# Kernel optimization log

Hardware: AMD Instinct MI355X
Metric: run time of the kernel (lower is better)

## Reference

```python
import jax, jax.numpy as jnp
import numpy as np

B, T, D_MODEL = 2, 2048, 1024
H, D_HEAD, R = 16, 64, 16
CAUSAL = True


def setup_inputs() -> dict:
    key = jax.random.key(0)
    ks = jax.random.split(key, 6)
    return {
        "x": jax.random.normal(ks[0], (B, T, D_MODEL), dtype=jnp.float32),
        "W_qkv": jax.random.normal(ks[1], (D_MODEL, 3 * D_MODEL), dtype=jnp.float32) * 0.02,
        "W_q_lsr": jax.random.normal(ks[2], (H, D_HEAD, R), dtype=jnp.float32) * 0.1,
        "W_k_lsr": jax.random.normal(ks[3], (H, D_HEAD, R), dtype=jnp.float32) * 0.1,
        "core": jax.random.normal(ks[4], (H, R), dtype=jnp.float32),
        "W_o": jax.random.normal(ks[5], (D_MODEL, D_MODEL), dtype=jnp.float32) * 0.02,
    }


def reference(x, W_qkv, W_q_lsr, W_k_lsr, core, W_o):
    Bx, Tx, D = x.shape
    Hh, Dh, Rr = W_q_lsr.shape
    # Fused QKV projection, then split heads -> (B, H, T, D_head)
    qkv = x @ W_qkv  # (B, T, 3D)
    q, k, v = jnp.split(qkv, 3, axis=-1)
    q = q.reshape(Bx, Tx, Hh, Dh).transpose(0, 2, 1, 3)
    k = k.reshape(Bx, Tx, Hh, Dh).transpose(0, 2, 1, 3)
    v = v.reshape(Bx, Tx, Hh, Dh).transpose(0, 2, 1, 3)
    # Low-rank (LSR) projections of q and k; core + 1/sqrt(R) scaling on q side
    scale = 1.0 / jnp.sqrt(jnp.asarray(max(Rr, 1), dtype=jnp.float32))
    q_lr = jnp.einsum('bhtd,hdr->bhtr', q, W_q_lsr) * core[None, :, None, :] * scale
    k_lr = jnp.einsum('bhtd,hdr->bhtr', k, W_k_lsr)
    # Low-rank scores (B, H, T, T)
    scores = jnp.einsum('bhir,bhjr->bhij', q_lr, k_lr)
    if CAUSAL:
        mask = jnp.tril(jnp.ones((Tx, Tx), dtype=bool))
        scores = jnp.where(mask[None, None], scores, -jnp.inf)
    attn = jax.nn.softmax(scores, axis=-1)
    out = jnp.einsum('bhij,bhjd->bhid', attn, v)  # (B, H, T, D_head)
    out = out.transpose(0, 2, 1, 3).reshape(Bx, Tx, D)
    return out @ W_o
```

## Files before the change

kernel.cpp:

```cpp
#include <hip/hip_runtime.h>
#include <hip/hip_bf16.h>

#define BB 2
#define TT 2048
#define DD 1024
#define HH 16
#define DH 64
#define RR 16
#define BT (BB*TT)
#define BH (BB*HH)
#define D3 (3*DD)
#define NC 1536

typedef __bf16 bf16x8 __attribute__((ext_vector_type(8)));
typedef float f32x4 __attribute__((ext_vector_type(4)));
typedef short short4v __attribute__((ext_vector_type(4)));

__device__ __forceinline__ float bf2f(unsigned short u) {
  unsigned int v = ((unsigned int)u) << 16;
  return __builtin_bit_cast(float, v);
}
__device__ __forceinline__ unsigned short f2bf(float f) {
  unsigned int x = __builtin_bit_cast(unsigned int, f);
  unsigned int r = x + 0x7fffu + ((x >> 16) & 1u);
  return (unsigned short)(r >> 16);
}
__device__ __forceinline__ short4v pack_bf16x4(float a, float b, float c, float d) {
  uint2 u;
  u.x = (unsigned)f2bf(a) | ((unsigned)f2bf(b) << 16);
  u.y = (unsigned)f2bf(c) | ((unsigned)f2bf(d) << 16);
  return __builtin_bit_cast(short4v, u);
}

#define NEG_BIG (-1e30f)

__device__ __forceinline__ void async_copy16(const void* g, void* l) {
  __builtin_amdgcn_global_load_lds((const __attribute__((address_space(1))) void*)g,
                                   (__attribute__((address_space(3))) void*)l, 16, 0, 0);
}

__global__ __launch_bounds__(256) void cvt_f32_bf16(const float* __restrict__ in,
                                                    unsigned short* __restrict__ out,
                                                    int n) {
  int i = (blockIdx.x * 256 + threadIdx.x) * 8;
  if (i >= n) return;
  float4 a = *(const float4*)&in[i];
  float4 b = *(const float4*)&in[i + 4];
  unsigned short t[8] = {f2bf(a.x), f2bf(a.y), f2bf(a.z), f2bf(a.w),
                         f2bf(b.x), f2bf(b.y), f2bf(b.z), f2bf(b.w)};
  *(uint4*)&out[i] = *(const uint4*)t;
}

__global__ __launch_bounds__(256) void transpose_cvt(const float* __restrict__ in,
                                                     unsigned short* __restrict__ out,
                                                     int R, int C, int coff) {
  __shared__ float tile[32][33];
  const int tx = threadIdx.x, ty = threadIdx.y;
  const int x = blockIdx.x * 32 + tx;
  const int y0 = blockIdx.y * 32;
#pragma unroll
  for (int i = 0; i < 32; i += 8)
    tile[ty + i][tx] = in[(size_t)(y0 + ty + i) * C + coff + x];
  __syncthreads();
  const int xo = y0 + tx;
  const int yo0 = blockIdx.x * 32;
#pragma unroll
  for (int i = 0; i < 32; i += 8)
    out[(size_t)(yo0 + ty + i) * R + xo] = f2bf(tile[tx][ty + i]);
}

__global__ __launch_bounds__(256) void build_lsr(const float* __restrict__ Wqkv,
                                                 const float* __restrict__ Wql,
                                                 const float* __restrict__ Wkl,
                                                 const float* __restrict__ core,
                                                 unsigned short* __restrict__ Wcomb_t) {
  const int d0 = blockIdx.x * 64, h = blockIdx.y, tid = threadIdx.x;
  __shared__ float Aq[64][65], Ak[64][65], Lq[64][16], Lk[64][16], cs[16];
#pragma unroll
  for (int p = 0; p < 16; p++) {
    int idx = p * 256 + tid, dd = idx >> 6, e = idx & 63;
    Aq[dd][e] = Wqkv[(size_t)(d0 + dd) * D3 + h * 64 + e];
    Ak[dd][e] = Wqkv[(size_t)(d0 + dd) * D3 + DD + h * 64 + e];
  }
#pragma unroll
  for (int p = 0; p < 4; p++) {
    int idx = p * 256 + tid, e = idx >> 4, r = idx & 15;
    Lq[e][r] = Wql[h * 1024 + e * 16 + r];
    Lk[e][r] = Wkl[h * 1024 + e * 16 + r];
  }
  if (tid < 16) cs[tid] = core[h * 16 + tid];
  __syncthreads();
  const int dd = tid & 63, rg = tid >> 6;
  float aq[4] = {}, ak[4] = {};
  for (int e = 0; e < 64; e++) {
    float xq = Aq[dd][e], xk = Ak[dd][e];
#pragma unroll
    for (int j = 0; j < 4; j++) {
      aq[j] += xq * Lq[e][rg * 4 + j];
      ak[j] += xk * Lk[e][rg * 4 + j];
    }
  }
#pragma unroll
  for (int j = 0; j < 4; j++) {
    int r = rg * 4 + j;
    Wcomb_t[(size_t)(1024 + h * 16 + r) * DD + d0 + dd] =
        f2bf(aq[j] * cs[r] * (0.25f * 1.4426950408889634f));
    Wcomb_t[(size_t)(1280 + h * 16 + r) * DD + d0 + dd] = f2bf(ak[j]);
  }
}

__device__ __forceinline__ void gemm64_core(const unsigned short* __restrict__ A,
                                            const unsigned short* __restrict__ Bt,
                                            int K, int bm, int bn,
                                            int tid, int g, int c, int wm, int wn,
                                            f32x4 acc[2][4]) {
  __shared__ __attribute__((aligned(16))) unsigned short As[2][64 * 32];
  __shared__ __attribute__((aligned(16))) unsigned short Bs[2][128 * 32];
  const int e0 = tid * 8;
  const int r0 = e0 >> 5, q0 = e0 & 31;
  const unsigned short* Arow = &A[(size_t)(bm * 64 + r0) * K + q0];
  const unsigned short* Brow0 = &Bt[(size_t)(bn * 128 + r0) * K + q0];
  const unsigned short* Brow1 = &Bt[(size_t)(bn * 128 + 64 + r0) * K + q0];
  async_copy16(Arow, &As[0][e0]);
  async_copy16(Brow0, &Bs[0][e0]);
  async_copy16(Brow1, &Bs[0][2048 + e0]);
  __syncthreads();
  const int nsteps = K >> 5;
#pragma unroll 2
  for (int t = 0; t < nsteps; t++) {
    const int cur = t & 1, nxt = cur ^ 1;
    if (t + 1 < nsteps) {
      const int k1 = (t + 1) << 5;
      async_copy16(Arow + k1, &As[nxt][e0]);
      async_copy16(Brow0 + k1, &Bs[nxt][e0]);
      async_copy16(Brow1 + k1, &Bs[nxt][2048 + e0]);
    }
    bf16x8 af[2];
#pragma unroll
    for (int mt = 0; mt < 2; mt++)
      af[mt] = *(const bf16x8*)&As[cur][(wm * 32 + mt * 16 + c) * 32 + g * 8];
#pragma unroll
    for (int nt = 0; nt < 4; nt++) {
      bf16x8 bf = *(const bf16x8*)&Bs[cur][(wn * 64 + nt * 16 + c) * 32 + g * 8];
#pragma unroll
      for (int mt = 0; mt < 2; mt++)
        acc[mt][nt] = __builtin_amdgcn_mfma_f32_16x16x32_bf16(af[mt], bf, acc[mt][nt], 0, 0, 0);
    }
    __syncthreads();
  }
}

__global__ __launch_bounds__(256) void gemm64_f32(const unsigned short* __restrict__ A,
                                                  const unsigned short* __restrict__ Bt,
                                                  float* __restrict__ C,
                                                  int M, int N, int K) {
  const int tid = threadIdx.x, lane = tid & 63;
  const int g = lane >> 4, c = lane & 15;
  const int wid = tid >> 6, wm = wid >> 1, wn = wid & 1;
  const int bm = blockIdx.y, bn = blockIdx.x;
  f32x4 acc[2][4] = {};
  gemm64_core(A, Bt, K, bm, bn, tid, g, c, wm, wn, acc);
#pragma unroll
  for (int mt = 0; mt < 2; mt++)
#pragma unroll
    for (int nt = 0; nt < 4; nt++)
#pragma unroll
      for (int r = 0; r < 4; r++) {
        int row = bm * 64 + wm * 32 + mt * 16 + g * 4 + r;
        int col = bn * 128 + wn * 64 + nt * 16 + c;
        C[(size_t)row * N + col] = acc[mt][nt][r];
      }
}

__global__ __launch_bounds__(256) void gemm_fused(const unsigned short* __restrict__ A,
                                                  const unsigned short* __restrict__ Bt,
                                                  unsigned short* __restrict__ qls,
                                                  unsigned short* __restrict__ klr,
                                                  unsigned short* __restrict__ vt,
                                                  int M, int N, int K) {
  const int tid = threadIdx.x, lane = tid & 63;
  const int g = lane >> 4, c = lane & 15;
  const int wid = tid >> 6, wm = wid >> 1, wn = wid & 1;
  const int bm = blockIdx.y, bn = blockIdx.x;
  f32x4 acc[2][4] = {};
  gemm64_core(A, Bt, K, bm, bn, tid, g, c, wm, wn, acc);
#pragma unroll
  for (int mt = 0; mt < 2; mt++)
#pragma unroll
    for (int nt = 0; nt < 4; nt++) {
      int colb = bn * 128 + wn * 64 + nt * 16;
      int tg0 = bm * 64 + wm * 32 + mt * 16 + g * 4;
      int b = tg0 >> 11, t0 = tg0 & 2047;
      if (colb < 1024) {
        int h = colb >> 6, d = (colb & 63) + c;
        uint2 pk = __builtin_bit_cast(uint2, pack_bf16x4(acc[mt][nt][0], acc[mt][nt][1],
                                                         acc[mt][nt][2], acc[mt][nt][3]));
        size_t idx = (size_t)(b * 16 + h) * (TT / 4) * 256 + (size_t)(t0 >> 2) * 256 + d * 4;
        *(uint2*)&vt[idx] = pk;
      } else if (colb < 1280) {
        int h = (colb - 1024) >> 4;
        size_t base = (size_t)(b * 16 + h) * TT;
#pragma unroll
        for (int r = 0; r < 4; r++)
          qls[(base + t0 + r) * 16 + c] = f2bf(acc[mt][nt][r]);
      } else {
        int h = (colb - 1280) >> 4;
        size_t base = (size_t)(b * 16 + h) * TT;
#pragma unroll
        for (int r = 0; r < 4; r++)
          klr[(base + t0 + r) * 16 + c] = f2bf(acc[mt][nt][r]);
      }
    }
}

__global__ __launch_bounds__(256, 3) void flash_lsr(const unsigned short* __restrict__ qls,
                                                    const unsigned short* __restrict__ klr,
                                                    const unsigned short* __restrict__ vt,
                                                    unsigned short* __restrict__ attn) {
  const int bh = blockIdx.x & 31, b = bh >> 4, h = bh & 15;
  const int qt = 31 - (blockIdx.x >> 5);
  const int tid = threadIdx.x, lane = tid & 63, w = tid >> 6;
  const int g = lane >> 4, c = lane & 15;
  const int q0 = qt * 64, jmax = qt >> 1;

  __shared__ __attribute__((aligned(16))) unsigned short Ks[2][128 * 20];
  __shared__ __attribute__((aligned(16))) unsigned short Vs[2][32 * 264];

  const size_t qbase = (size_t)bh * TT;
  const short4v qf = __builtin_bit_cast(short4v,
      *(const uint2*)&qls[(qbase + q0 + w * 16 + c) * 16 + g * 4]);
  const int qg = q0 + w * 16 + c;
  float mi = NEG_BIG, li = 0.f;
  f32x4 oa[4] = {};
  const f32x4 zero = {0.f, 0.f, 0.f, 0.f};
  const size_t kb = (size_t)bh * TT * 16;
  const size_t vb = (size_t)bh * TT * 64;
  const int srcl = g * 20;

  uint4 kr = *(const uint4*)&klr[kb + tid * 8];
  uint4 vr[4];
#pragma unroll
  for (int p = 0; p < 4; p++)
    vr[p] = *(const uint4*)&vt[vb + (p * 256 + tid) * 8];

  int p = 0;
  f32x4 s[8];
  for (int jt = 0; jt <= jmax; jt++) {
    *(uint4*)&Ks[p][(tid >> 1) * 20 + (tid & 1) * 8] = kr;
#pragma unroll
    for (int q = 0; q < 4; q++) {
      int e = (q * 256 + tid) * 8;
      *(uint4*)&Vs[p][(e >> 8) * 264 + (e & 255)] = vr[q];
    }
    __syncthreads();
    if (jt < jmax) {
      kr = *(const uint4*)&klr[kb + (size_t)(jt + 1) * 2048 + tid * 8];
      const unsigned short* vp = &vt[vb + (size_t)(jt + 1) * 8192];
#pragma unroll
      for (int q = 0; q < 4; q++)
        vr[q] = *(const uint4*)&vp[(q * 256 + tid) * 8];
    }
    const unsigned short* Kb = Ks[p];
#pragma unroll
    for (int nt = 0; nt < 8; nt++) {
      short4v kf = __builtin_bit_cast(short4v, *(const uint2*)&Kb[(nt * 16 + c) * 20 + g * 4]);
      s[nt] = __builtin_amdgcn_mfma_f32_16x16x16bf16_1k(kf, qf, zero, 0, 0, 0);
    }
    if (jt == jmax) {
#pragma unroll
      for (int nt = 0; nt < 8; nt++)
#pragma unroll
        for (int r = 0; r < 4; r++) {
          int jg = jt * 128 + nt * 16 + g * 4 + r;
          if (jg > qg) s[nt][r] = NEG_BIG;
        }
    }
    f32x4 vm = s[0];
#pragma unroll
    for (int nt = 1; nt < 8; nt++)
#pragma unroll
      for (int r = 0; r < 4; r++) vm[r] = fmaxf(vm[r], s[nt][r]);
    float rm = fmaxf(fmaxf(vm[0], vm[1]), fmaxf(vm[2], vm[3]));
    rm = fmaxf(rm, __shfl_xor(rm, 16, 64));
    rm = fmaxf(rm, __shfl_xor(rm, 32, 64));
    float mnew = fmaxf(mi, rm);
    float alpha = __builtin_amdgcn_exp2f(mi - mnew);
    mi = mnew;
    f32x4 vs = zero;
#pragma unroll
    for (int nt = 0; nt < 8; nt++)
#pragma unroll
      for (int r = 0; r < 4; r++) {
        float pv = __builtin_amdgcn_exp2f(s[nt][r] - mnew);
        s[nt][r] = pv;
        vs[r] += pv;
      }
    float rs = (vs[0] + vs[1]) + (vs[2] + vs[3]);
    rs += __shfl_xor(rs, 16, 64);
    rs += __shfl_xor(rs, 32, 64);
    li = li * alpha + rs;
    float av[4];
#pragma unroll
    for (int r = 0; r < 4; r++) av[r] = __shfl(alpha, srcl + r, 64);
#pragma unroll
    for (int nd = 0; nd < 4; nd++)
#pragma unroll
      for (int r = 0; r < 4; r++) oa[nd][r] *= av[r];
    const unsigned short* Vb = Vs[p];
#pragma unroll
    for (int kc = 0; kc < 8; kc++) {
      short4v af = pack_bf16x4(s[kc][0], s[kc][1], s[kc][2], s[kc][3]);
#pragma unroll
      for (int nd = 0; nd < 4; nd++) {
        uint2 vv = *(const uint2*)&Vb[(kc * 4 + g) * 264 + (nd * 16 + c) * 4];
        short4v vf = __builtin_bit_cast(short4v, vv);
        oa[nd] = __builtin_amdgcn_mfma_f32_16x16x16bf16_1k(af, vf, oa[nd], 0, 0, 0);
      }
    }
    p ^= 1;
  }

  float inv = 1.f / li;
  float iv[4];
#pragma unroll
  for (int r = 0; r < 4; r++) iv[r] = __shfl(inv, srcl + r, 64);
#pragma unroll
  for (int r = 0; r < 4; r++) {
    size_t rowb = ((size_t)b * TT + q0 + w * 16 + g * 4 + r) * DD + h * 64;
#pragma unroll
    for (int nd = 0; nd < 4; nd++)
      attn[rowb + nd * 16 + c] = f2bf(oa[nd][r] * iv[r]);
  }
}

extern "C" void kernel_launch(void* const* d_in, const int* in_sizes, int n_in,
                              void* d_out, int out_size, void* d_ws, size_t ws_size,
                              hipStream_t stream) {
  const float* x      = (const float*)d_in[0];
  const float* W_qkv  = (const float*)d_in[1];
  const float* W_qlsr = (const float*)d_in[2];
  const float* W_klsr = (const float*)d_in[3];
  const float* core   = (const float*)d_in[4];
  const float* W_o    = (const float*)d_in[5];
  float* out = (float*)d_out;

  char* ws = (char*)d_ws;
  unsigned short* x_bf    = (unsigned short*)ws; ws += (size_t)BT * DD * 2;
  unsigned short* Wcomb_t = (unsigned short*)ws; ws += (size_t)NC * DD * 2;
  unsigned short* Wo_t    = (unsigned short*)ws; ws += (size_t)DD * DD * 2;
  unsigned short* qls     = (unsigned short*)ws; ws += (size_t)BH * TT * 16 * 2;
  unsigned short* klr     = (unsigned short*)ws; ws += (size_t)BH * TT * 16 * 2;
  unsigned short* vt      = (unsigned short*)ws; ws += (size_t)BH * TT * 64 * 2;
  unsigned short* attn    = (unsigned short*)ws; ws += (size_t)BT * DD * 2;

  cvt_f32_bf16<<<(BT * DD) / (256 * 8), 256, 0, stream>>>(x, x_bf, BT * DD);
  transpose_cvt<<<dim3(32, 32), dim3(32, 8), 0, stream>>>(W_o, Wo_t, DD, DD, 0);
  transpose_cvt<<<dim3(32, 32), dim3(32, 8), 0, stream>>>(W_qkv, Wcomb_t, DD, D3, 2048);
  build_lsr<<<dim3(16, 16), 256, 0, stream>>>(W_qkv, W_qlsr, W_klsr, core, Wcomb_t);
  gemm_fused<<<dim3(NC / 128, BT / 64), 256, 0, stream>>>(x_bf, Wcomb_t, qls, klr, vt, BT, NC, DD);
  flash_lsr<<<dim3(32 * BH), 256, 0, stream>>>(qls, klr, vt, attn);
  gemm64_f32<<<dim3(DD / 128, BT / 64), 256, 0, stream>>>(attn, Wo_t, out, BT, DD, DD);
}
```

Before: 188.4 us.

## Fuse prep kernels into one launch and transpose PV MFMA to drop shuffles

Merges the x conversion, the two weight transposes and the LSR weight build into a single launch that branches on block index, removing three launch gaps. In the flash kernel the PV MFMA operands are swapped so each lane owns whole rows of the output. This removes the cross-lane shuffles for the alpha rescale and the final normalisation, and lets the output be written as packed 4-element stores. It also switches to hardware bf16 conversion for packing. The fused prep kernel allocates the larger shared-memory footprint for every block, which may lower occupancy on the simple conversion blocks.

```diff
diff --git a/kernel.cpp b/kernel.cpp
--- a/kernel.cpp
+++ b/kernel.cpp
@@ -13,6 +13,7 @@
 #define NC 1536
 
 typedef __bf16 bf16x8 __attribute__((ext_vector_type(8)));
+typedef __bf16 bf16x4 __attribute__((ext_vector_type(4)));
 typedef float f32x4 __attribute__((ext_vector_type(4)));
 typedef short short4v __attribute__((ext_vector_type(4)));
 
@@ -31,6 +32,10 @@
   u.y = (unsigned)f2bf(c) | ((unsigned)f2bf(d) << 16);
   return __builtin_bit_cast(short4v, u);
 }
+__device__ __forceinline__ short4v pack4_cvt(float a, float b, float c, float d) {
+  bf16x4 v = {(__bf16)a, (__bf16)b, (__bf16)c, (__bf16)d};
+  return __builtin_bit_cast(short4v, v);
+}
 
 #define NEG_BIG (-1e30f)
 
@@ -39,73 +44,74 @@
                                    (__attribute__((address_space(3))) void*)l, 16, 0, 0);
 }
 
-__global__ __launch_bounds__(256) void cvt_f32_bf16(const float* __restrict__ in,
-                                                    unsigned short* __restrict__ out,
-                                                    int n) {
-  int i = (blockIdx.x * 256 + threadIdx.x) * 8;
-  if (i >= n) return;
-  float4 a = *(const float4*)&in[i];
-  float4 b = *(const float4*)&in[i + 4];
-  unsigned short t[8] = {f2bf(a.x), f2bf(a.y), f2bf(a.z), f2bf(a.w),
-                         f2bf(b.x), f2bf(b.y), f2bf(b.z), f2bf(b.w)};
-  *(uint4*)&out[i] = *(const uint4*)t;
-}
-
-__global__ __launch_bounds__(256) void transpose_cvt(const float* __restrict__ in,
-                                                     unsigned short* __restrict__ out,
-                                                     int R, int C, int coff) {
+__global__ __launch_bounds__(256) void prep_fused(const float* __restrict__ x,
+                                                  const float* __restrict__ Wqkv,
+                                                  const float* __restrict__ Wql,
+                                                  const float* __restrict__ Wkl,
+                                                  const float* __restrict__ core,
+                                                  const float* __restrict__ Wo,
+                                                  unsigned short* __restrict__ x_bf,
+                                                  unsigned short* __restrict__ Wcomb_t,
+                                                  unsigned short* __restrict__ Wo_t) {
   __shared__ float tile[32][33];
-  const int tx = threadIdx.x, ty = threadIdx.y;
-  const int x = blockIdx.x * 32 + tx;
-  const int y0 = blockIdx.y * 32;
-#pragma unroll
-  for (int i = 0; i < 32; i += 8)
-    tile[ty + i][tx] = in[(size_t)(y0 + ty + i) * C + coff + x];
-  __syncthreads();
-  const int xo = y0 + tx;
-  const int yo0 = blockIdx.x * 32;
-#pragma unroll
-  for (int i = 0; i < 32; i += 8)
-    out[(size_t)(yo0 + ty + i) * R + xo] = f2bf(tile[tx][ty + i]);
-}
-
-__global__ __launch_bounds__(256) void build_lsr(const float* __restrict__ Wqkv,
-                                                 const float* __restrict__ Wql,
-                                                 const float* __restrict__ Wkl,
-                                                 const float* __restrict__ core,
-                                                 unsigned short* __restrict__ Wcomb_t) {
-  const int d0 = blockIdx.x * 64, h = blockIdx.y, tid = threadIdx.x;
   __shared__ float Aq[64][65], Ak[64][65], Lq[64][16], Lk[64][16], cs[16];
-#pragma unroll
-  for (int p = 0; p < 16; p++) {
-    int idx = p * 256 + tid, dd = idx >> 6, e = idx & 63;
-    Aq[dd][e] = Wqkv[(size_t)(d0 + dd) * D3 + h * 64 + e];
-    Ak[dd][e] = Wqkv[(size_t)(d0 + dd) * D3 + DD + h * 64 + e];
-  }
-#pragma unroll
-  for (int p = 0; p < 4; p++) {
-    int idx = p * 256 + tid, e = idx >> 4, r = idx & 15;
-    Lq[e][r] = Wql[h * 1024 + e * 16 + r];
-    Lk[e][r] = Wkl[h * 1024 + e * 16 + r];
-  }
-  if (tid < 16) cs[tid] = core[h * 16 + tid];
-  __syncthreads();
-  const int dd = tid & 63, rg = tid >> 6;
-  float aq[4] = {}, ak[4] = {};
-  for (int e = 0; e < 64; e++) {
-    float xq = Aq[dd][e], xk = Ak[dd][e];
+  const int bid = blockIdx.x, tid = threadIdx.x;
+  if (bid < 2048) {
+    int i = (bid * 256 + tid) * 8;
+    float4 a = *(const float4*)&x[i];
+    float4 b = *(const float4*)&x[i + 4];
+    unsigned short t[8] = {f2bf(a.x), f2bf(a.y), f2bf(a.z), f2bf(a.w),
+                           f2bf(b.x), f2bf(b.y), f2bf(b.z), f2bf(b.w)};
+    *(uint4*)&x_bf[i] = *(const uint4*)t;
+  } else if (bid < 4096) {
+    const float* in; unsigned short* out; int C, coff, lb;
+    if (bid < 3072) { in = Wo;   out = Wo_t;    C = DD; coff = 0;    lb = bid - 2048; }
+    else            { in = Wqkv; out = Wcomb_t; C = D3; coff = 2048; lb = bid - 3072; }
+    const int tx = tid & 31, ty = tid >> 5;
+    const int bx = lb & 31, by = lb >> 5;
+    const int xx = bx * 32 + tx, y0 = by * 32;
+#pragma unroll
+    for (int i = 0; i < 32; i += 8)
+      tile[ty + i][tx] = in[(size_t)(y0 + ty + i) * C + coff + xx];
+    __syncthreads();
+    const int xo = y0 + tx, yo0 = bx * 32;
+#pragma unroll
+    for (int i = 0; i < 32; i += 8)
+      out[(size_t)(yo0 + ty + i) * DD + xo] = f2bf(tile[tx][ty + i]);
+  } else {
+    const int l = bid - 4096;
+    const int d0 = (l & 15) * 64, h = l >> 4;
+#pragma unroll
+    for (int p = 0; p < 16; p++) {
+      int idx = p * 256 + tid, dd = idx >> 6, e = idx & 63;
+      Aq[dd][e] = Wqkv[(size_t)(d0 + dd) * D3 + h * 64 + e];
+      Ak[dd][e] = Wqkv[(size_t)(d0 + dd) * D3 + DD + h * 64 + e];
+    }
+#pragma unroll
+    for (int p = 0; p < 4; p++) {
+      int idx = p * 256 + tid, e = idx >> 4, r = idx & 15;
+      Lq[e][r] = Wql[h * 1024 + e * 16 + r];
+      Lk[e][r] = Wkl[h * 1024 + e * 16 + r];
+    }
+    if (tid < 16) cs[tid] = core[h * 16 + tid];
+    __syncthreads();
+    const int dd = tid & 63, rg = tid >> 6;
+    float aq[4] = {}, ak[4] = {};
+    for (int e = 0; e < 64; e++) {
+      float xq = Aq[dd][e], xk = Ak[dd][e];
+#pragma unroll
+      for (int j = 0; j < 4; j++) {
+        aq[j] += xq * Lq[e][rg * 4 + j];
+        ak[j] += xk * Lk[e][rg * 4 + j];
+      }
+    }
 #pragma unroll
     for (int j = 0; j < 4; j++) {
-      aq[j] += xq * Lq[e][rg * 4 + j];
-      ak[j] += xk * Lk[e][rg * 4 + j];
-    }
-  }
-#pragma unroll
-  for (int j = 0; j < 4; j++) {
-    int r = rg * 4 + j;
-    Wcomb_t[(size_t)(1024 + h * 16 + r) * DD + d0 + dd] =
-        f2bf(aq[j] * cs[r] * (0.25f * 1.4426950408889634f));
-    Wcomb_t[(size_t)(1280 + h * 16 + r) * DD + d0 + dd] = f2bf(ak[j]);
+      int r = rg * 4 + j;
+      Wcomb_t[(size_t)(1024 + h * 16 + r) * DD + d0 + dd] =
+          f2bf(aq[j] * cs[r] * (0.25f * 1.4426950408889634f));
+      Wcomb_t[(size_t)(1280 + h * 16 + r) * DD + d0 + dd] = f2bf(ak[j]);
+    }
   }
 }
 
@@ -235,7 +241,6 @@
   const f32x4 zero = {0.f, 0.f, 0.f, 0.f};
   const size_t kb = (size_t)bh * TT * 16;
   const size_t vb = (size_t)bh * TT * 64;
-  const int srcl = g * 20;
 
   uint4 kr = *(const uint4*)&klr[kb + tid * 8];
   uint4 vr[4];
@@ -299,37 +304,31 @@
     rs += __shfl_xor(rs, 16, 64);
     rs += __shfl_xor(rs, 32, 64);
     li = li * alpha + rs;
-    float av[4];
-#pragma unroll
-    for (int r = 0; r < 4; r++) av[r] = __shfl(alpha, srcl + r, 64);
 #pragma unroll
     for (int nd = 0; nd < 4; nd++)
 #pragma unroll
-      for (int r = 0; r < 4; r++) oa[nd][r] *= av[r];
+      for (int r = 0; r < 4; r++) oa[nd][r] *= alpha;
     const unsigned short* Vb = Vs[p];
 #pragma unroll
     for (int kc = 0; kc < 8; kc++) {
-      short4v af = pack_bf16x4(s[kc][0], s[kc][1], s[kc][2], s[kc][3]);
+      short4v pf = pack4_cvt(s[kc][0], s[kc][1], s[kc][2], s[kc][3]);
 #pragma unroll
       for (int nd = 0; nd < 4; nd++) {
         uint2 vv = *(const uint2*)&Vb[(kc * 4 + g) * 264 + (nd * 16 + c) * 4];
         short4v vf = __builtin_bit_cast(short4v, vv);
-        oa[nd] = __builtin_amdgcn_mfma_f32_16x16x16bf16_1k(af, vf, oa[nd], 0, 0, 0);
+        oa[nd] = __builtin_amdgcn_mfma_f32_16x16x16bf16_1k(vf, pf, oa[nd], 0, 0, 0);
       }
     }
     p ^= 1;
   }
 
-  float inv = 1.f / li;
-  float iv[4];
-#pragma unroll
-  for (int r = 0; r < 4; r++) iv[r] = __shfl(inv, srcl + r, 64);
-#pragma unroll
-  for (int r = 0; r < 4; r++) {
-    size_t rowb = ((size_t)b * TT + q0 + w * 16 + g * 4 + r) * DD + h * 64;
-#pragma unroll
-    for (int nd = 0; nd < 4; nd++)
-      attn[rowb + nd * 16 + c] = f2bf(oa[nd][r] * iv[r]);
+  const float inv = 1.f / li;
+  const size_t rowb = ((size_t)b * TT + q0 + w * 16 + c) * DD + h * 64;
+#pragma unroll
+  for (int nd = 0; nd < 4; nd++) {
+    short4v pk = pack4_cvt(oa[nd][0] * inv, oa[nd][1] * inv,
+                           oa[nd][2] * inv, oa[nd][3] * inv);
+    *(uint2*)&attn[rowb + nd * 16 + g * 4] = __builtin_bit_cast(uint2, pk);
   }
 }
 
@@ -353,10 +352,8 @@
   unsigned short* vt      = (unsigned short*)ws; ws += (size_t)BH * TT * 64 * 2;
   unsigned short* attn    = (unsigned short*)ws; ws += (size_t)BT * DD * 2;
 
-  cvt_f32_bf16<<<(BT * DD) / (256 * 8), 256, 0, stream>>>(x, x_bf, BT * DD);
-  transpose_cvt<<<dim3(32, 32), dim3(32, 8), 0, stream>>>(W_o, Wo_t, DD, DD, 0);
-  transpose_cvt<<<dim3(32, 32), dim3(32, 8), 0, stream>>>(W_qkv, Wcomb_t, DD, D3, 2048);
-  build_lsr<<<dim3(16, 16), 256, 0, stream>>>(W_qkv, W_qlsr, W_klsr, core, Wcomb_t);
+  prep_fused<<<4352, 256, 0, stream>>>(x, W_qkv, W_qlsr, W_klsr, core, W_o,
+                                       x_bf, Wcomb_t, Wo_t);
   gemm_fused<<<dim3(NC / 128, BT / 64), 256, 0, stream>>>(x_bf, Wcomb_t, qls, klr, vt, BT, NC, DD);
   flash_lsr<<<dim3(32 * BH), 256, 0, stream>>>(qls, klr, vt, attn);
   gemm64_f32<<<dim3(DD / 128, BT / 64), 256, 0, stream>>>(attn, Wo_t, out, BT, DD, DD);
```

After: 185.9 us. Within noise of the previous version (-1.3%).
